# Kernel optimization log

Measured on AMD Instinct MI355X. Metric: run time of the kernel, lower is better.

## Reference

```python
import jax, jax.numpy as jnp
import numpy as np
import math

B, S, D, H = 2, 2048, 1024, 16
DH = D // H  # head_dim = 64
NEG = -10000.0


def setup_inputs() -> dict:
    key = jax.random.key(0)
    ks = jax.random.split(key, 6)
    scale = 1.0 / math.sqrt(D)
    inp = {
        "query": jax.random.normal(ks[0], (B, S, D), dtype=jnp.float32),
        "key": jax.random.normal(ks[1], (B, S, D), dtype=jnp.float32),
        "value": jax.random.normal(ks[2], (B, S, D), dtype=jnp.float32),
        "Wq": jax.random.normal(ks[3], (D, D), dtype=jnp.float32) * scale,
        "Wk": jax.random.normal(ks[4], (D, D), dtype=jnp.float32) * scale,
        "Wv": jax.random.normal(ks[5], (D, D), dtype=jnp.float32) * scale,
        "pad_mask": jnp.ones((B, 1, 1, S), dtype=jnp.int32),
        "attn_mask": jnp.tril(jnp.ones((S, S), dtype=jnp.int32))[None, None],  # causal [1,1,S,S]
    }
    return inp


def reference(query, key, value, Wq, Wk, Wv, pad_mask, attn_mask):
    b, s, d = query.shape
    # torch Linear(bias=False): y = x @ W.T ; then split into heads [B,H,S,DH]
    def proj(x, W):
        return (x @ W.T).reshape(b, -1, H, DH).transpose(0, 2, 1, 3)

    Q = proj(query, Wq)
    K = proj(key, Wk)
    V = proj(value, Wv)

    scores = jnp.einsum("bhqd,bhkd->bhqk", Q, K) / math.sqrt(DH)
    scores = jnp.where(attn_mask == 0, NEG, scores)
    scores = jnp.where(pad_mask == 0, NEG, scores)
    attn = jax.nn.softmax(scores, axis=-1)  # dropout p=0.0 -> identity
    ctx = jnp.einsum("bhqk,bhkd->bhqd", attn, V)
    return ctx.transpose(0, 2, 1, 3).reshape(b, -1, d)
```

## Files before the change

kernel.cpp:

```cpp
#include <hip/hip_runtime.h>


typedef unsigned short u16;
typedef unsigned int u32;
typedef u16 u16x4 __attribute__((ext_vector_type(4)));
typedef u16 u16x8 __attribute__((ext_vector_type(8)));
typedef u32 u32x2 __attribute__((ext_vector_type(2)));
typedef u32 u32x4 __attribute__((ext_vector_type(4)));
typedef __bf16 bf16x8 __attribute__((ext_vector_type(8)));
typedef float f32x4 __attribute__((ext_vector_type(4)));

static __device__ __forceinline__ u16 f2bf(float f) {
  unsigned u = __builtin_bit_cast(unsigned, f);
  return (u16)((u + 0x7FFFu + ((u >> 16) & 1u)) >> 16);
}

static __device__ __forceinline__ u32 cvt_pk_bf16(float lo, float hi) {
  u32 r;
  asm("v_cvt_pk_bf16_f32 %0, %1, %2" : "=v"(r) : "v"(lo), "v"(hi));
  return r;
}

static __device__ __forceinline__ u16x8 cvt8(float4 f0, float4 f1) {
  u32x4 v;
  v[0] = cvt_pk_bf16(f0.x, f0.y);
  v[1] = cvt_pk_bf16(f0.z, f0.w);
  v[2] = cvt_pk_bf16(f1.x, f1.y);
  v[3] = cvt_pk_bf16(f1.z, f1.w);
  return __builtin_bit_cast(u16x8, v);
}

static __device__ __forceinline__ f32x4 mfma16(u16x8 a, u16x8 b, f32x4 c) {
  return __builtin_amdgcn_mfma_f32_16x16x32_bf16(
      __builtin_bit_cast(bf16x8, a), __builtin_bit_cast(bf16x8, b), c, 0, 0, 0);
}

static __device__ __forceinline__ float bperm_f(int lane, float v) {
  return __builtin_bit_cast(
      float, __builtin_amdgcn_ds_bpermute(lane * 4, __builtin_bit_cast(int, v)));
}

#define GLOAD16(GSRC, LDST)                                                  \
  __builtin_amdgcn_global_load_lds(                                         \
      (const __attribute__((address_space(1))) unsigned int*)(GSRC),        \
      (__attribute__((address_space(3))) unsigned int*)(LDST), 16, 0, 0)

#define FENCE() asm volatile("" ::: "memory")
#define BARX()                        \
  do {                                \
    __builtin_amdgcn_s_barrier();     \
    FENCE();                          \
  } while (0)

__global__ __launch_bounds__(256) void wconv_kernel(
    const float* __restrict__ Wq, const float* __restrict__ Wk,
    const float* __restrict__ Wv, u16* __restrict__ dst) {
  const float* src = (blockIdx.y == 0) ? Wq : (blockIdx.y == 1) ? Wk : Wv;
  u16* d = dst + (size_t)blockIdx.y * (1024 * 1024);
  const int i = (blockIdx.x * 256 + threadIdx.x) * 8;
  const float4 f0 = *(const float4*)(src + i);
  const float4 f1 = *(const float4*)(src + i + 4);
  *(u16x8*)(d + i) = cvt8(f0, f1);
}

__global__ __launch_bounds__(256) void proj_kernel(
    const float* __restrict__ Xq, const float* __restrict__ Xk, const float* __restrict__ Xv,
    const u16* __restrict__ Wbf,
    u16* __restrict__ Qb, u16* __restrict__ Kb, u16* __restrict__ Vt) {
  const int d0 = blockIdx.x;
  const int tid = (d0 & 7) * 96 + (d0 >> 3);
  const int nI = tid % 24, mI = tid / 24;
  const int mode = nI >> 3;
  const int m0 = mI * 128;
  const int n0 = (nI & 7) * 128;

  const float* __restrict__ X = (mode == 0) ? Xq : (mode == 1) ? Xk : Xv;
  const u16* __restrict__ W = Wbf + (size_t)mode * (1024 * 1024);

  __shared__ __align__(16) char As[3][128 * 128];
  __shared__ __align__(16) char Bs[3][128 * 64];

  const int t = threadIdx.x;
  const int lane = t & 63;
  const int w = t >> 6;
  const int wm = w >> 1, wn = w & 1;
  const int lr = lane & 15, lg = lane >> 4;

  const float* aptr[4];
  int aoff[4];
#pragma unroll
  for (int jj = 0; jj < 4; ++jj) {
    const int j = w * 4 + jj;
    aptr[jj] = X + (size_t)(m0 + j * 8 + (lane >> 3)) * 1024 +
               ((lane & 7) ^ (lane >> 3)) * 4;
    aoff[jj] = j * 1024;
  }
  const u16* bptr[2];
  int boff[2];
#pragma unroll
  for (int jj = 0; jj < 2; ++jj) {
    const int j = w * 2 + jj;
    bptr[jj] = W + (size_t)(n0 + j * 16 + (lane >> 2)) * 1024 +
               ((lane & 3) ^ ((lane >> 3) & 3)) * 8;
    boff[jj] = j * 1024;
  }

#define ISSUE(T, BUF)                                            \
  do {                                                           \
    _Pragma("unroll") for (int jj = 0; jj < 4; ++jj)             \
        GLOAD16(aptr[jj] + (size_t)(T) * 32, As[BUF] + aoff[jj]); \
    _Pragma("unroll") for (int jj = 0; jj < 2; ++jj)             \
        GLOAD16(bptr[jj] + (size_t)(T) * 32, Bs[BUF] + boff[jj]); \
  } while (0)

  f32x4 acc[4][4] = {};

#define CMP(BUF)                                                              \
  do {                                                                       \
    u16x8 af[4], bfr[4];                                                     \
    _Pragma("unroll") for (int mi = 0; mi < 4; ++mi) {                        \
      const int row = wm * 64 + mi * 16 + lr;                                \
      const int rs = row & 7;                                                \
      const f32x4 c0 =                                                       \
          *(const f32x4*)(As[BUF] + row * 128 + (((lg * 2) ^ rs) * 16));     \
      const f32x4 c1 =                                                       \
          *(const f32x4*)(As[BUF] + row * 128 + (((lg * 2 + 1) ^ rs) * 16)); \
      u32x4 pk;                                                              \
      pk[0] = cvt_pk_bf16(c0[0], c0[1]);                                     \
      pk[1] = cvt_pk_bf16(c0[2], c0[3]);                                     \
      pk[2] = cvt_pk_bf16(c1[0], c1[1]);                                     \
      pk[3] = cvt_pk_bf16(c1[2], c1[3]);                                     \
      af[mi] = __builtin_bit_cast(u16x8, pk);                                \
    }                                                                         \
    _Pragma("unroll") for (int ni = 0; ni < 4; ++ni) {                        \
      const int row = wn * 64 + ni * 16 + lr;                                \
      bfr[ni] = *(const u16x8*)(Bs[BUF] + row * 64 +                         \
                                ((lg ^ ((row >> 1) & 3)) * 16));             \
    }                                                                         \
    _Pragma("unroll") for (int mi = 0; mi < 4; ++mi)                          \
        _Pragma("unroll") for (int ni = 0; ni < 4; ++ni)                      \
            acc[mi][ni] = mfma16(af[mi], bfr[ni], acc[mi][ni]);               \
  } while (0)

  ISSUE(0, 0);
  ISSUE(1, 1);
  ISSUE(2, 2);
  asm volatile("s_waitcnt vmcnt(12)" ::: "memory");
  BARX();

  for (int tt = 0; tt < 29; ++tt) {
    CMP(tt % 3);
    asm volatile("s_waitcnt lgkmcnt(0)" ::: "memory");
    BARX();
    ISSUE(tt + 3, tt % 3);
    asm volatile("s_waitcnt vmcnt(12)" ::: "memory");
    BARX();
  }
  CMP(29 % 3);
  asm volatile("s_waitcnt vmcnt(6)" ::: "memory");
  BARX();
  CMP(30 % 3);
  asm volatile("s_waitcnt vmcnt(0)" ::: "memory");
  BARX();
  CMP(31 % 3);
#undef ISSUE
#undef CMP

#pragma unroll
  for (int mi = 0; mi < 4; ++mi) {
    const int sbase = m0 + wm * 64 + mi * 16 + lg * 4;
    const int b_ = sbase >> 11;
    const int s_ = sbase & 2047;
#pragma unroll
    for (int ni = 0; ni < 4; ++ni) {
      const int n = n0 + wn * 64 + ni * 16 + lr;
      const int h_ = n >> 6, dh = n & 63;
      if (mode == 2) {
        u16x4 pk;
        pk[0] = f2bf(acc[mi][ni][0]);
        pk[1] = f2bf(acc[mi][ni][1]);
        pk[2] = f2bf(acc[mi][ni][2]);
        pk[3] = f2bf(acc[mi][ni][3]);
        *(u16x4*)(Vt + ((size_t)((b_ * 16 + h_) * 64 + dh)) * 2048 + s_) = pk;
      } else {
        const float sc = (mode == 0) ? 0.18033688f : 1.0f;
        u16* dst = (mode == 0 ? Qb : Kb) + (size_t)(b_ * 16 + h_) * (2048 * 64) + dh;
#pragma unroll
        for (int r = 0; r < 4; ++r)
          dst[(size_t)(s_ + r) * 64] = f2bf(acc[mi][ni][r] * sc);
      }
    }
  }
}

__global__ __launch_bounds__(256, 2) void attn_kernel(
    const u16* __restrict__ Qb, const u16* __restrict__ Kb, const u16* __restrict__ Vt,
    const int* __restrict__ pad, float* __restrict__ out) {
  const int id = blockIdx.x;
  const int g = id >> 8, r_ = id & 255;
  const int bh = r_ & 31;
  const int p8 = r_ >> 5;
  const int pi = g ? (15 - p8) : p8;
  const int qbA = 31 - pi, qbB = pi;

  const int b = bh >> 4, h = bh & 15;
  const u16* Qh = Qb + (size_t)bh * (2048 * 64);
  const u16* Kh = Kb + (size_t)bh * (2048 * 64);
  const u16* Vh = Vt + (size_t)bh * (64 * 2048);
  const int* padb = pad + b * 2048;

  __shared__ u16 Ks[2][64 * 64];
  __shared__ u16 Vs[2][64 * 64];
  __shared__ u16 Ps[4][16 * 64];

  const int t = threadIdx.x, lane = t & 63, w = t >> 6;
  const int lr = lane & 15, lg = lane >> 4;
  const int swz = (lr & 7) << 4;
  const int sr = t >> 3, scb = t & 7;
  const int qwaveA = qbA * 64 + w * 16, qwaveB = qbB * 64 + w * 16;

  u16x8 qfA[2], qfB[2];
#pragma unroll
  for (int kc = 0; kc < 2; ++kc) {
    qfA[kc] = *(const u16x8*)(Qh + (size_t)(qwaveA + lr) * 64 + kc * 32 + lg * 8);
    qfB[kc] = *(const u16x8*)(Qh + (size_t)(qwaveB + lr) * 64 + kc * 32 + lg * 8);
  }

  f32x4 accA[4] = {}, accB[4] = {};
  float mrowA = -1e4f, lsumA = 0.f, mrowB = -1e4f, lsumB = 0.f;

  u16x8 kr0, kr1, vr0, vr1;
  const int sb0 = (sr * 128 + scb * 16) ^ ((sr & 7) << 4);
  const int sb1 = ((32 + sr) * 128 + scb * 16) ^ ((sr & 7) << 4);

  kr0 = *(const u16x8*)(Kh + (size_t)sr * 64 + scb * 8);
  kr1 = *(const u16x8*)(Kh + (size_t)(32 + sr) * 64 + scb * 8);
  vr0 = *(const u16x8*)(Vh + (size_t)sr * 2048 + scb * 8);
  vr1 = *(const u16x8*)(Vh + (size_t)(32 + sr) * 2048 + scb * 8);
  *(u16x8*)((char*)Ks[0] + sb0) = kr0;
  *(u16x8*)((char*)Ks[0] + sb1) = kr1;
  *(u16x8*)((char*)Vs[0] + sb0) = vr0;
  *(u16x8*)((char*)Vs[0] + sb1) = vr1;
  __syncthreads();

#define PROCESS(QF, ACC, MROW, LSUM, QWAVE)                                    \
  do {                                                                         \
    f32x4 s4[4] = {};                                                          \
    __builtin_amdgcn_s_setprio(1);                                             \
    _Pragma("unroll") for (int ct = 0; ct < 4; ++ct) {                         \
      if (kv0 + ct * 16 <= (QWAVE) + 15) {                                     \
        _Pragma("unroll") for (int kc = 0; kc < 2; ++kc) {                     \
          const int byt = ((ct * 16 + lr) * 128 + kc * 64 + lg * 16) ^ swz;    \
          const u16x8 kf = *(const u16x8*)((char*)KsC + byt);                  \
          s4[ct] = mfma16(kf, QF[kc], s4[ct]);                                 \
        }                                                                      \
      }                                                                        \
    }                                                                          \
    __builtin_amdgcn_s_setprio(0);                                             \
    float vv[4][4];                                                            \
    if ((kv0 + 63 <= (QWAVE)) && allpad) {                                     \
      _Pragma("unroll") for (int ct = 0; ct < 4; ++ct)                         \
          _Pragma("unroll") for (int rr = 0; rr < 4; ++rr)                     \
              vv[ct][rr] = s4[ct][rr];                                         \
    } else {                                                                   \
      const int lim = (QWAVE) + lr - kv0 - lg * 4;                             \
      _Pragma("unroll") for (int ct = 0; ct < 4; ++ct) {                       \
        const int* pvp = (const int*)&pv4[ct];                                 \
        _Pragma("unroll") for (int rr = 0; rr < 4; ++rr)                       \
            vv[ct][rr] = (pvp[rr] && (ct * 16 + rr) <= lim) ? s4[ct][rr]       \
                                                            : -1e4f;           \
      }                                                                        \
    }                                                                          \
    float m0_ = fmaxf(fmaxf(fmaxf(vv[0][0], vv[0][1]), fmaxf(vv[0][2], vv[0][3])), \
                      fmaxf(fmaxf(vv[1][0], vv[1][1]), fmaxf(vv[1][2], vv[1][3]))); \
    float m1_ = fmaxf(fmaxf(fmaxf(vv[2][0], vv[2][1]), fmaxf(vv[2][2], vv[2][3])), \
                      fmaxf(fmaxf(vv[3][0], vv[3][1]), fmaxf(vv[3][2], vv[3][3]))); \
    float mx = fmaxf(m0_, m1_);                                                \
    mx = fmaxf(mx, __shfl_xor(mx, 16));                                        \
    mx = fmaxf(mx, __shfl_xor(mx, 32));                                        \
    if (!__all(mx <= (MROW) + 8.0f)) { \
      const float mn = fmaxf((MROW), mx);                                      \
      const float al = exp2f((MROW) - mn);                                     \
      (MROW) = mn;                                                             \
      (LSUM) *= al;                                                            \
      _Pragma("unroll") for (int rr = 0; rr < 4; ++rr) {                       \
        const float alv = bperm_f(lg * 4 + rr, al);                            \
        _Pragma("unroll") for (int dt = 0; dt < 4; ++dt) ACC[dt][rr] *= alv;   \
      }                                                                        \
    }                                                                          \
    float p[4][4];                                                             \
    _Pragma("unroll") for (int ct = 0; ct < 4; ++ct)                           \
        _Pragma("unroll") for (int rr = 0; rr < 4; ++rr)                       \
            p[ct][rr] = exp2f(vv[ct][rr] - (MROW));                            \
    float ps = (((p[0][0] + p[0][1]) + (p[0][2] + p[0][3])) +                  \
                ((p[1][0] + p[1][1]) + (p[1][2] + p[1][3]))) +                 \
               (((p[2][0] + p[2][1]) + (p[2][2] + p[2][3])) +                  \
                ((p[3][0] + p[3][1]) + (p[3][2] + p[3][3])));                  \
    ps += __shfl_xor(ps, 16);                                                  \
    ps += __shfl_xor(ps, 32);                                                  \
    (LSUM) += ps;                                                              \
    u16* PsB = &Ps[w][0];                                                      \
    _Pragma("unroll") for (int ct = 0; ct < 4; ++ct) {                         \
      u32x2 pw;                                                                \
      pw[0] = cvt_pk_bf16(p[ct][0], p[ct][1]);                                 \
      pw[1] = cvt_pk_bf16(p[ct][2], p[ct][3]);                                 \
      const int pb = (lr * 128 + ct * 32 + lg * 8) ^ swz;                      \
      *(u32x2*)((char*)PsB + pb) = pw;                                         \
    }                                                                          \
    const u16x8 pa0 = *(const u16x8*)((char*)PsB + ((lr * 128 + lg * 16) ^ swz));      \
    const u16x8 pa1 = *(const u16x8*)((char*)PsB + ((lr * 128 + 64 + lg * 16) ^ swz)); \
    __builtin_amdgcn_s_setprio(1);                                             \
    _Pragma("unroll") for (int dt = 0; dt < 4; ++dt) {                         \
      const int r0 = (dt * 16 + lr) * 128;                                     \
      ACC[dt] = mfma16(pa0, *(const u16x8*)((char*)VsC + ((r0 + lg * 16) ^ swz)), ACC[dt]);      \
      ACC[dt] = mfma16(pa1, *(const u16x8*)((char*)VsC + ((r0 + 64 + lg * 16) ^ swz)), ACC[dt]); \
    }                                                                          \
    __builtin_amdgcn_s_setprio(0);                                             \
  } while (0)

  int cur = 0;
  const int nst = qbA + 1;
  for (int st = 0; st < nst; ++st) {
    const int kv0 = st << 6;
    const bool more = st + 1 < nst;
    if (more) {
      const int nv0 = kv0 + 64;
      kr0 = *(const u16x8*)(Kh + (size_t)(nv0 + sr) * 64 + scb * 8);
      kr1 = *(const u16x8*)(Kh + (size_t)(nv0 + 32 + sr) * 64 + scb * 8);
      vr0 = *(const u16x8*)(Vh + (size_t)sr * 2048 + nv0 + scb * 8);
      vr1 = *(const u16x8*)(Vh + (size_t)(32 + sr) * 2048 + nv0 + scb * 8);
    }
    int4 pv4[4];
#pragma unroll
    for (int ct = 0; ct < 4; ++ct)
      pv4[ct] = *(const int4*)(padb + kv0 + ct * 16 + lg * 4);
    const int pall = pv4[0].x & pv4[0].y & pv4[0].z & pv4[0].w &
                     pv4[1].x & pv4[1].y & pv4[1].z & pv4[1].w &
                     pv4[2].x & pv4[2].y & pv4[2].z & pv4[2].w &
                     pv4[3].x & pv4[3].y & pv4[3].z & pv4[3].w;
    const bool allpad = __all(pall != 0);

    const u16* KsC = Ks[cur];
    const u16* VsC = Vs[cur];

    PROCESS(qfA, accA, mrowA, lsumA, qwaveA);
    if (st <= qbB)
      PROCESS(qfB, accB, mrowB, lsumB, qwaveB);

    if (more) {
      u16* Kn = Ks[cur ^ 1];
      u16* Vn = Vs[cur ^ 1];
      *(u16x8*)((char*)Kn + sb0) = kr0;
      *(u16x8*)((char*)Kn + sb1) = kr1;
      *(u16x8*)((char*)Vn + sb0) = vr0;
      *(u16x8*)((char*)Vn + sb1) = vr1;
    }
    __syncthreads();
    cur ^= 1;
  }
#undef PROCESS

#pragma unroll
  for (int tile = 0; tile < 2; ++tile) {
    const f32x4* acc = tile ? accB : accA;
    const float lsum = tile ? lsumB : lsumA;
    const int qwave = tile ? qwaveB : qwaveA;
    const float il = 1.0f / lsum;
    float* obase = out + ((size_t)(b * 2048 + qwave + lg * 4)) * 1024 + h * 64 + lr;
#pragma unroll
    for (int r = 0; r < 4; ++r) {
      const float linv = bperm_f(lg * 4 + r, il);
#pragma unroll
      for (int dt = 0; dt < 4; ++dt)
        obase[(size_t)r * 1024 + dt * 16] = acc[dt][r] * linv;
    }
  }
}

extern "C" void kernel_launch(void* const* d_in, const int* in_sizes, int n_in,
                              void* d_out, int out_size, void* d_ws, size_t ws_size,
                              hipStream_t stream) {
  const float* q  = (const float*)d_in[0];
  const float* k  = (const float*)d_in[1];
  const float* v  = (const float*)d_in[2];
  const float* wq = (const float*)d_in[3];
  const float* wk = (const float*)d_in[4];
  const float* wv = (const float*)d_in[5];
  const int* pad  = (const int*)d_in[6];
  float* out = (float*)d_out;

  u16* Qb  = (u16*)d_ws;
  u16* Kb  = Qb + (size_t)4 * 1024 * 1024;
  u16* Vt  = Kb + (size_t)4 * 1024 * 1024;
  u16* Wbf = Vt + (size_t)4 * 1024 * 1024;

  dim3 gc(512, 3);
  wconv_kernel<<<gc, 256, 0, stream>>>(wq, wk, wv, Wbf);

  proj_kernel<<<768, 256, 0, stream>>>(q, k, v, Wbf, Qb, Kb, Vt);

  attn_kernel<<<512, 256, 0, stream>>>(Qb, Kb, Vt, pad, out);
}
```

Before: 110.3 us.

## Pre-convert activations to bf16 in a separate pass before projection GEMM

The weight-conversion kernel is extended into a combined conversion kernel that also casts the fp32 query/key/value activations to bf16 in workspace. The projection GEMM then streams bf16 activations straight into LDS. This halves its A-tile LDS footprint and global traffic, and removes the per-tile fp32-to-bf16 packing, with wait counts adjusted to the smaller load count. In exchange it adds a full extra read and write pass over the activations, needs more workspace, and drops the XOR swizzle on the LDS tiles, which may introduce bank conflicts.

```diff
diff --git a/kernel.cpp b/kernel.cpp
--- a/kernel.cpp
+++ b/kernel.cpp
@@ -52,20 +52,26 @@
     FENCE();                          \
   } while (0)
 
-__global__ __launch_bounds__(256) void wconv_kernel(
-    const float* __restrict__ Wq, const float* __restrict__ Wk,
-    const float* __restrict__ Wv, u16* __restrict__ dst) {
-  const float* src = (blockIdx.y == 0) ? Wq : (blockIdx.y == 1) ? Wk : Wv;
-  u16* d = dst + (size_t)blockIdx.y * (1024 * 1024);
-  const int i = (blockIdx.x * 256 + threadIdx.x) * 8;
+__global__ __launch_bounds__(256) void cvt_kernel(
+    const float* __restrict__ Xq, const float* __restrict__ Xk,
+    const float* __restrict__ Xv, const float* __restrict__ Wq,
+    const float* __restrict__ Wk, const float* __restrict__ Wv,
+    u16* __restrict__ Xb, u16* __restrict__ Wb) {
+  const int y = blockIdx.y;
+  const float* src = (y == 0) ? Xq : (y == 1) ? Xk : (y == 2) ? Xv
+                   : (y == 3) ? Wq : (y == 4) ? Wk : Wv;
+  const size_t nelem = (y < 3) ? (size_t)4 * 1024 * 1024 : (size_t)1024 * 1024;
+  u16* dst = (y < 3) ? Xb + (size_t)y * 4 * 1024 * 1024
+                     : Wb + (size_t)(y - 3) * 1024 * 1024;
+  const size_t i = ((size_t)blockIdx.x * 256 + threadIdx.x) * 8;
+  if (i >= nelem) return;
   const float4 f0 = *(const float4*)(src + i);
   const float4 f1 = *(const float4*)(src + i + 4);
-  *(u16x8*)(d + i) = cvt8(f0, f1);
+  *(u16x8*)(dst + i) = cvt8(f0, f1);
 }
 
 __global__ __launch_bounds__(256) void proj_kernel(
-    const float* __restrict__ Xq, const float* __restrict__ Xk, const float* __restrict__ Xv,
-    const u16* __restrict__ Wbf,
+    const u16* __restrict__ Xbf, const u16* __restrict__ Wbf,
     u16* __restrict__ Qb, u16* __restrict__ Kb, u16* __restrict__ Vt) {
   const int d0 = blockIdx.x;
   const int tid = (d0 & 7) * 96 + (d0 >> 3);
@@ -74,10 +80,10 @@
   const int m0 = mI * 128;
   const int n0 = (nI & 7) * 128;
 
-  const float* __restrict__ X = (mode == 0) ? Xq : (mode == 1) ? Xk : Xv;
+  const u16* __restrict__ X = Xbf + (size_t)mode * (4 * 1024 * 1024);
   const u16* __restrict__ W = Wbf + (size_t)mode * (1024 * 1024);
 
-  __shared__ __align__(16) char As[3][128 * 128];
+  __shared__ __align__(16) char As[3][128 * 64];
   __shared__ __align__(16) char Bs[3][128 * 64];
 
   const int t = threadIdx.x;
@@ -86,31 +92,25 @@
   const int wm = w >> 1, wn = w & 1;
   const int lr = lane & 15, lg = lane >> 4;
 
-  const float* aptr[4];
-  int aoff[4];
-#pragma unroll
-  for (int jj = 0; jj < 4; ++jj) {
-    const int j = w * 4 + jj;
-    aptr[jj] = X + (size_t)(m0 + j * 8 + (lane >> 3)) * 1024 +
-               ((lane & 7) ^ (lane >> 3)) * 4;
-    aoff[jj] = j * 1024;
-  }
+  const u16* aptr[2];
   const u16* bptr[2];
-  int boff[2];
+  int soff[2];
 #pragma unroll
   for (int jj = 0; jj < 2; ++jj) {
     const int j = w * 2 + jj;
-    bptr[jj] = W + (size_t)(n0 + j * 16 + (lane >> 2)) * 1024 +
-               ((lane & 3) ^ ((lane >> 3) & 3)) * 8;
-    boff[jj] = j * 1024;
-  }
-
-#define ISSUE(T, BUF)                                            \
-  do {                                                           \
-    _Pragma("unroll") for (int jj = 0; jj < 4; ++jj)             \
-        GLOAD16(aptr[jj] + (size_t)(T) * 32, As[BUF] + aoff[jj]); \
-    _Pragma("unroll") for (int jj = 0; jj < 2; ++jj)             \
-        GLOAD16(bptr[jj] + (size_t)(T) * 32, Bs[BUF] + boff[jj]); \
+    const int row = j * 16 + (lane >> 2);
+    const int col = (lane & 3) * 8;
+    aptr[jj] = X + (size_t)(m0 + row) * 1024 + col;
+    bptr[jj] = W + (size_t)(n0 + row) * 1024 + col;
+    soff[jj] = j * 1024;
+  }
+
+#define ISSUE(T, BUF)                                                \
+  do {                                                               \
+    _Pragma("unroll") for (int jj = 0; jj < 2; ++jj)                 \
+        GLOAD16(aptr[jj] + (size_t)(T) * 32, As[BUF] + soff[jj]);    \
+    _Pragma("unroll") for (int jj = 0; jj < 2; ++jj)                 \
+        GLOAD16(bptr[jj] + (size_t)(T) * 32, Bs[BUF] + soff[jj]);    \
   } while (0)
 
   f32x4 acc[4][4] = {};
@@ -120,22 +120,11 @@
     u16x8 af[4], bfr[4];                                                     \
     _Pragma("unroll") for (int mi = 0; mi < 4; ++mi) {                        \
       const int row = wm * 64 + mi * 16 + lr;                                \
-      const int rs = row & 7;                                                \
-      const f32x4 c0 =                                                       \
-          *(const f32x4*)(As[BUF] + row * 128 + (((lg * 2) ^ rs) * 16));     \
-      const f32x4 c1 =                                                       \
-          *(const f32x4*)(As[BUF] + row * 128 + (((lg * 2 + 1) ^ rs) * 16)); \
-      u32x4 pk;                                                              \
-      pk[0] = cvt_pk_bf16(c0[0], c0[1]);                                     \
-      pk[1] = cvt_pk_bf16(c0[2], c0[3]);                                     \
-      pk[2] = cvt_pk_bf16(c1[0], c1[1]);                                     \
-      pk[3] = cvt_pk_bf16(c1[2], c1[3]);                                     \
-      af[mi] = __builtin_bit_cast(u16x8, pk);                                \
+      af[mi] = *(const u16x8*)(As[BUF] + row * 64 + lg * 16);                \
     }                                                                         \
     _Pragma("unroll") for (int ni = 0; ni < 4; ++ni) {                        \
       const int row = wn * 64 + ni * 16 + lr;                                \
-      bfr[ni] = *(const u16x8*)(Bs[BUF] + row * 64 +                         \
-                                ((lg ^ ((row >> 1) & 3)) * 16));             \
+      bfr[ni] = *(const u16x8*)(Bs[BUF] + row * 64 + lg * 16);               \
     }                                                                         \
     _Pragma("unroll") for (int mi = 0; mi < 4; ++mi)                          \
         _Pragma("unroll") for (int ni = 0; ni < 4; ++ni)                      \
@@ -145,7 +134,7 @@
   ISSUE(0, 0);
   ISSUE(1, 1);
   ISSUE(2, 2);
-  asm volatile("s_waitcnt vmcnt(12)" ::: "memory");
+  asm volatile("s_waitcnt vmcnt(8)" ::: "memory");
   BARX();
 
   for (int tt = 0; tt < 29; ++tt) {
@@ -153,11 +142,11 @@
     asm volatile("s_waitcnt lgkmcnt(0)" ::: "memory");
     BARX();
     ISSUE(tt + 3, tt % 3);
-    asm volatile("s_waitcnt vmcnt(12)" ::: "memory");
+    asm volatile("s_waitcnt vmcnt(8)" ::: "memory");
     BARX();
   }
   CMP(29 % 3);
-  asm volatile("s_waitcnt vmcnt(6)" ::: "memory");
+  asm volatile("s_waitcnt vmcnt(4)" ::: "memory");
   BARX();
   CMP(30 % 3);
   asm volatile("s_waitcnt vmcnt(0)" ::: "memory");
@@ -393,11 +382,12 @@
   u16* Kb  = Qb + (size_t)4 * 1024 * 1024;
   u16* Vt  = Kb + (size_t)4 * 1024 * 1024;
   u16* Wbf = Vt + (size_t)4 * 1024 * 1024;
-
-  dim3 gc(512, 3);
-  wconv_kernel<<<gc, 256, 0, stream>>>(wq, wk, wv, Wbf);
-
-  proj_kernel<<<768, 256, 0, stream>>>(q, k, v, Wbf, Qb, Kb, Vt);
+  u16* Xbf = Wbf + (size_t)3 * 1024 * 1024;
+
+  dim3 gv(2048, 6);
+  cvt_kernel<<<gv, 256, 0, stream>>>(q, k, v, wq, wk, wv, Xbf, Wbf);
+
+  proj_kernel<<<768, 256, 0, stream>>>(Xbf, Wbf, Qb, Kb, Vt);
 
   attn_kernel<<<512, 256, 0, stream>>>(Qb, Kb, Vt, pad, out);
 }
```

Result: faster. 106.0 us (-3.9%).
